# Kernel optimization log

Measured on AMD Instinct MI355X. Metric: run time of the kernel, lower is better.

## Reference

```python
import jax, jax.numpy as jnp
import numpy as np

N = 50000
E = 800000
D_IN = 64
D_E = 32
H = 128
EPS = 1e-5


def _seg_mean(msgs, dst, n):
    s = jax.ops.segment_sum(msgs, dst, num_segments=n)
    c = jax.ops.segment_sum(jnp.ones((dst.shape[0], 1), msgs.dtype), dst, num_segments=n)
    return s / jnp.maximum(c, 1.0)


def _bn(h, g, b, m, v):
    return g * (h - m) * jax.lax.rsqrt(v + EPS) + b


def setup_inputs() -> dict:
    key = jax.random.key(0)
    ks = jax.random.split(key, 32)
    inp = {
        "x": jax.random.normal(ks[0], (N, D_IN), jnp.float32),
        "edge_index_0": jax.random.randint(ks[1], (2, E), 0, N),
        "edge_index_1": jax.random.randint(ks[2], (2, E), 0, N),
        "edge_index_2": jax.random.randint(ks[3], (2, E), 0, N),
        "edge_attr_0": jax.random.normal(ks[4], (E, D_E), jnp.float32),
        # conv1: Linear(D_IN + D_E -> H)
        "W1": jax.random.normal(ks[5], (H, D_IN + D_E), jnp.float32) * 0.1,
        "b1": jnp.zeros((H,), jnp.float32),
        "g1": jnp.ones((H,), jnp.float32), "be1": jnp.zeros((H,), jnp.float32),
        "m1": jax.random.normal(ks[6], (H,), jnp.float32) * 0.1,
        "v1": jax.random.uniform(ks[7], (H,), jnp.float32) + 0.5,
        # SAGEConv2: lin_l (bias) on aggregated neighbors + lin_r (no bias) on self
        "Wl2": jax.random.normal(ks[8], (H, H), jnp.float32) * 0.1,
        "bl2": jnp.zeros((H,), jnp.float32),
        "Wr2": jax.random.normal(ks[9], (H, H), jnp.float32) * 0.1,
        "g2": jnp.ones((H,), jnp.float32), "be2": jnp.zeros((H,), jnp.float32),
        "m2": jax.random.normal(ks[10], (H,), jnp.float32) * 0.1,
        "v2": jax.random.uniform(ks[11], (H,), jnp.float32) + 0.5,
        # SAGEConv3
        "Wl3": jax.random.normal(ks[12], (H, H), jnp.float32) * 0.1,
        "bl3": jnp.zeros((H,), jnp.float32),
        "Wr3": jax.random.normal(ks[13], (H, H), jnp.float32) * 0.1,
        "g3": jnp.ones((H,), jnp.float32), "be3": jnp.zeros((H,), jnp.float32),
        "m3": jax.random.normal(ks[14], (H,), jnp.float32) * 0.1,
        "v3": jax.random.uniform(ks[15], (H,), jnp.float32) + 0.5,
        # mlp: Linear(H + D_IN -> 64) -> ReLU -> Linear(64 -> 1)
        "W4": jax.random.normal(ks[16], (64, H + D_IN), jnp.float32) * 0.1,
        "b4": jnp.zeros((64,), jnp.float32),
        "W5": jax.random.normal(ks[17], (1, 64), jnp.float32) * 0.1,
        "b5": jnp.zeros((1,), jnp.float32),
    }
    return inp


def reference(x, edge_index_0, edge_index_1, edge_index_2, edge_attr_0,
              W1, b1, g1, be1, m1, v1,
              Wl2, bl2, Wr2, g2, be2, m2, v2,
              Wl3, bl3, Wr3, g3, be3, m3, v3,
              W4, b4, W5, b5):
    n = x.shape[0]
    init = x
    # conv1: gather x_j + edge_attr, concat, linear, mean scatter, relu (update)
    msg = jnp.concatenate([x[edge_index_0[0]], edge_attr_0], axis=-1) @ W1.T + b1  # [E,H]
    h = jax.nn.relu(_seg_mean(msg, edge_index_0[1], n))
    h = jax.nn.relu(_bn(h, g1, be1, m1, v1))  # dropout: eval (identity)
    # conv2: SAGEConv = lin_l(mean_j x_j) + lin_r(x)
    agg = _seg_mean(h[edge_index_1[0]], edge_index_1[1], n)
    h = agg @ Wl2.T + bl2 + h @ Wr2.T
    h = jax.nn.relu(_bn(h, g2, be2, m2, v2))
    # conv3
    agg = _seg_mean(h[edge_index_2[0]], edge_index_2[1], n)
    h = agg @ Wl3.T + bl3 + h @ Wr3.T
    h = jax.nn.relu(_bn(h, g3, be3, m3, v3))
    # readout mlp on [h, initial_embedding]
    z = jnp.concatenate([h, init], axis=1)
    z = jax.nn.relu(z @ W4.T + b4)
    out = (z @ W5.T + b5).squeeze(-1)  # [N]
    return out
```

## Files before the change

### kernel.cpp

```cpp
#include <hip/hip_runtime.h>
#include <hip/hip_bf16.h>
#include <stdint.h>

#define NN 50000
#define NE 800000
#define EPS 1e-5f

#define KB 196
#define SH 8
#define NPB 256
#define RCAP 4500
#define PT2 2048

typedef __attribute__((ext_vector_type(8))) short bf16x8;
typedef __attribute__((ext_vector_type(4))) float floatx4;

static __device__ __forceinline__ float bf2f(unsigned int u){
  union { unsigned int i; float f; } c; c.i = u << 16; return c.f;
}
static __device__ __forceinline__ unsigned short f2bf(float f){
  union { float f; unsigned int i; } c; c.f = f;
  unsigned int x = c.i;
  return (unsigned short)((x + 0x7fffu + ((x >> 16) & 1u)) >> 16);
}

#define CVT_X   3200000
#define CVT_W1  3212288
#define CVT_WL2 3228672
#define CVT_WR2 3245056
#define CVT_WL3 3261440
#define CVT_WR3 3277824
#define CVT_END 3290112
__global__ void k_cvt_all(const float* __restrict__ x,  const float* __restrict__ W1,
                          const float* __restrict__ Wl2, const float* __restrict__ Wr2,
                          const float* __restrict__ Wl3, const float* __restrict__ Wr3,
                          const float* __restrict__ W4,
                          unsigned short* __restrict__ xb,  unsigned short* __restrict__ W1b,
                          unsigned short* __restrict__ Wl2b, unsigned short* __restrict__ Wr2b,
                          unsigned short* __restrict__ Wl3b, unsigned short* __restrict__ Wr3b,
                          unsigned short* __restrict__ W4b, int* __restrict__ gcur){
  int i = blockIdx.x * 256 + threadIdx.x;
  if(i >= CVT_END) return;
  if(i < 3 * KB) gcur[i] = 0;
  if(i < CVT_X)        xb[i] = f2bf(x[i]);
  else if(i < CVT_W1)  W1b[i - CVT_X]    = f2bf(W1[i - CVT_X]);
  else if(i < CVT_WL2) Wl2b[i - CVT_W1]  = f2bf(Wl2[i - CVT_W1]);
  else if(i < CVT_WR2) Wr2b[i - CVT_WL2] = f2bf(Wr2[i - CVT_WL2]);
  else if(i < CVT_WL3) Wl3b[i - CVT_WR2] = f2bf(Wl3[i - CVT_WR2]);
  else if(i < CVT_WR3) Wr3b[i - CVT_WL3] = f2bf(Wr3[i - CVT_WL3]);
  else                 W4b[i - CVT_WR3]  = f2bf(W4[i - CVT_WR3]);
}

__global__ void k_part0(const int* __restrict__ ei, int* __restrict__ gcur,
                        int2* __restrict__ rec, int* __restrict__ recE){
  __shared__ int2 stage[PT2];
  __shared__ int stE[PT2];
  __shared__ int hist[KB], ex[KB], cur[KB], gbase[KB];
  __shared__ int part[256];
  __shared__ int tot;
  int tid = threadIdx.x;
  int tile = blockIdx.x * PT2;
  for(int i = tid; i < KB; i += 256) hist[i] = 0;
  __syncthreads();
  int dst[8], src[8];
  #pragma unroll
  for(int j = 0; j < 8; j++){
    int e = tile + j * 256 + tid;
    if(e < NE){ src[j] = ei[e]; dst[j] = ei[NE + e]; atomicAdd(&hist[dst[j] >> SH], 1); }
    else dst[j] = -1;
  }
  __syncthreads();
  int c0 = (tid < KB) ? hist[tid] : 0;
  part[tid] = c0;
  __syncthreads();
  for(int d = 1; d < 256; d <<= 1){
    int v = (tid >= d) ? part[tid - d] : 0;
    __syncthreads();
    part[tid] += v;
    __syncthreads();
  }
  if(tid < KB){
    int e = part[tid] - c0;
    ex[tid] = e; cur[tid] = e;
    gbase[tid] = atomicAdd(&gcur[tid], c0);
  }
  if(tid == 255) tot = part[255];
  __syncthreads();
  #pragma unroll
  for(int j = 0; j < 8; j++){
    if(dst[j] >= 0){
      int b = dst[j] >> SH;
      int s = atomicAdd(&cur[b], 1);
      stage[s] = make_int2(dst[j], src[j]);
      stE[s] = tile + j * 256 + tid;
    }
  }
  __syncthreads();
  for(int s = tid; s < tot; s += 256){
    int2 r = stage[s];
    int b = r.x >> SH;
    int idx = b * RCAP + gbase[b] + (s - ex[b]);
    rec[idx] = r;
    recE[idx] = stE[s];
  }
}

__global__ void k_part(const int* __restrict__ ei, int* __restrict__ gcur, int2* __restrict__ rec){
  __shared__ int2 stage[PT2];
  __shared__ int hist[KB], ex[KB], cur[KB], gbase[KB];
  __shared__ int part[256];
  __shared__ int tot;
  int tid = threadIdx.x;
  int tile = blockIdx.x * PT2;
  for(int i = tid; i < KB; i += 256) hist[i] = 0;
  __syncthreads();
  int dst[8], src[8];
  #pragma unroll
  for(int j = 0; j < 8; j++){
    int e = tile + j * 256 + tid;
    if(e < NE){ src[j] = ei[e]; dst[j] = ei[NE + e]; atomicAdd(&hist[dst[j] >> SH], 1); }
    else dst[j] = -1;
  }
  __syncthreads();
  int c0 = (tid < KB) ? hist[tid] : 0;
  part[tid] = c0;
  __syncthreads();
  for(int d = 1; d < 256; d <<= 1){
    int v = (tid >= d) ? part[tid - d] : 0;
    __syncthreads();
    part[tid] += v;
    __syncthreads();
  }
  if(tid < KB){
    int e = part[tid] - c0;
    ex[tid] = e; cur[tid] = e;
    gbase[tid] = atomicAdd(&gcur[tid], c0);
  }
  if(tid == 255) tot = part[255];
  __syncthreads();
  #pragma unroll
  for(int j = 0; j < 8; j++){
    if(dst[j] >= 0){
      int b = dst[j] >> SH;
      int s = atomicAdd(&cur[b], 1);
      stage[s] = make_int2(dst[j], src[j]);
    }
  }
  __syncthreads();
  for(int s = tid; s < tot; s += 256){
    int2 r = stage[s];
    int b = r.x >> SH;
    rec[b * RCAP + gbase[b] + (s - ex[b])] = r;
  }
}

__global__ void k_build0(const int2* __restrict__ rec, const int* __restrict__ recE,
                         const int* __restrict__ gcnt,
                         int2* __restrict__ adj2, int* __restrict__ rowbeg, int* __restrict__ deg){
  __shared__ int cnt[NPB], cur2[NPB];
  __shared__ int part[256];
  int b = blockIdx.x, tid = threadIdx.x;
  int n0 = b << SH;
  int nr = gcnt[b];
  const int2* r = rec + b * RCAP;
  const int* re = recE + b * RCAP;
  cnt[tid] = 0;
  __syncthreads();
  for(int k = tid; k < nr; k += 256) atomicAdd(&cnt[r[k].x - n0], 1);
  __syncthreads();
  int c0 = cnt[tid];
  part[tid] = c0;
  __syncthreads();
  for(int d = 1; d < 256; d <<= 1){
    int v = (tid >= d) ? part[tid - d] : 0;
    __syncthreads();
    part[tid] += v;
    __syncthreads();
  }
  int base = part[tid] - c0;
  cur2[tid] = base;
  __syncthreads();
  int n = n0 + tid;
  if(n < NN){ rowbeg[n] = b * RCAP + base; deg[n] = c0; }
  for(int k = tid; k < nr; k += 256){
    int2 q = r[k];
    int p = atomicAdd(&cur2[q.x - n0], 1);
    adj2[b * RCAP + p] = make_int2(q.y, re[k]);
  }
}

__global__ void k_build(const int2* __restrict__ rec, const int* __restrict__ gcnt,
                        int* __restrict__ adj, int* __restrict__ rowbeg, int* __restrict__ deg){
  __shared__ int cnt[NPB], cur2[NPB];
  __shared__ int part[256];
  int b = blockIdx.x, tid = threadIdx.x;
  int n0 = b << SH;
  int nr = gcnt[b];
  const int2* r = rec + b * RCAP;
  cnt[tid] = 0;
  __syncthreads();
  for(int k = tid; k < nr; k += 256) atomicAdd(&cnt[r[k].x - n0], 1);
  __syncthreads();
  int c0 = cnt[tid];
  part[tid] = c0;
  __syncthreads();
  for(int d = 1; d < 256; d <<= 1){
    int v = (tid >= d) ? part[tid - d] : 0;
    __syncthreads();
    part[tid] += v;
    __syncthreads();
  }
  int base = part[tid] - c0;
  cur2[tid] = base;
  __syncthreads();
  int n = n0 + tid;
  if(n < NN){ rowbeg[n] = b * RCAP + base; deg[n] = c0; }
  for(int k = tid; k < nr; k += 256){
    int2 q = r[k];
    int p = atomicAdd(&cur2[q.x - n0], 1);
    adj[b * RCAP + p] = q.y;
  }
}

__global__ void k_aggXE(const int* __restrict__ rowbeg, const int* __restrict__ deg,
                        const int2* __restrict__ adj2,
                        const unsigned short* __restrict__ xb, const float* __restrict__ ea,
                        unsigned short* __restrict__ agg){
  int w = (blockIdx.x * blockDim.x + threadIdx.x) >> 6;
  int lane = threadIdx.x & 63;
  if(w >= NN) return;
  int sub = lane >> 4, li = lane & 15;
  int r0 = rowbeg[w], dg = deg[w], r1 = r0 + dg;
  float acc[8] = {0.f,0.f,0.f,0.f,0.f,0.f,0.f,0.f};
  for(int k = r0; k < r1; k += 8){
    int e0 = k + sub, e1 = k + 4 + sub;
    int i0 = e0 < r1 ? e0 : r1 - 1;
    int i1 = e1 < r1 ? e1 : r1 - 1;
    float m0 = e0 < r1 ? 1.f : 0.f;
    float m1 = e1 < r1 ? 1.f : 0.f;
    int2 a0 = adj2[i0], a1 = adj2[i1];
    if(li < 8){
      uint4 v0 = *(const uint4*)(xb + (size_t)a0.x * 64 + li * 8);
      uint4 v1 = *(const uint4*)(xb + (size_t)a1.x * 64 + li * 8);
      acc[0] += m0 * bf2f(v0.x & 0xffffu); acc[1] += m0 * bf2f(v0.x >> 16);
      acc[2] += m0 * bf2f(v0.y & 0xffffu); acc[3] += m0 * bf2f(v0.y >> 16);
      acc[4] += m0 * bf2f(v0.z & 0xffffu); acc[5] += m0 * bf2f(v0.z >> 16);
      acc[6] += m0 * bf2f(v0.w & 0xffffu); acc[7] += m0 * bf2f(v0.w >> 16);
      acc[0] += m1 * bf2f(v1.x & 0xffffu); acc[1] += m1 * bf2f(v1.x >> 16);
      acc[2] += m1 * bf2f(v1.y & 0xffffu); acc[3] += m1 * bf2f(v1.y >> 16);
      acc[4] += m1 * bf2f(v1.z & 0xffffu); acc[5] += m1 * bf2f(v1.z >> 16);
      acc[6] += m1 * bf2f(v1.w & 0xffffu); acc[7] += m1 * bf2f(v1.w >> 16);
    } else {
      int j = li - 8;
      float4 p0 = *(const float4*)(ea + (size_t)a0.y * 32 + j * 4);
      float4 p1 = *(const float4*)(ea + (size_t)a1.y * 32 + j * 4);
      acc[0] += m0 * p0.x; acc[1] += m0 * p0.y;
      acc[2] += m0 * p0.z; acc[3] += m0 * p0.w;
      acc[0] += m1 * p1.x; acc[1] += m1 * p1.y;
      acc[2] += m1 * p1.z; acc[3] += m1 * p1.w;
    }
  }
  #pragma unroll
  for(int d = 16; d < 64; d <<= 1){
    #pragma unroll
    for(int i = 0; i < 8; i++) acc[i] += __shfl_xor(acc[i], d, 64);
  }
  if(sub == 0){
    float inv = 1.0f / (float)(dg > 0 ? dg : 1);
    if(li < 8){
      unsigned int q0 = (unsigned int)f2bf(acc[0]*inv) | ((unsigned int)f2bf(acc[1]*inv) << 16);
      unsigned int q1 = (unsigned int)f2bf(acc[2]*inv) | ((unsigned int)f2bf(acc[3]*inv) << 16);
      unsigned int q2 = (unsigned int)f2bf(acc[4]*inv) | ((unsigned int)f2bf(acc[5]*inv) << 16);
      unsigned int q3 = (unsigned int)f2bf(acc[6]*inv) | ((unsigned int)f2bf(acc[7]*inv) << 16);
      *(uint4*)(agg + (size_t)w * 96 + li * 8) = make_uint4(q0, q1, q2, q3);
    } else {
      int j = li - 8;
      unsigned int q0 = (unsigned int)f2bf(acc[0]*inv) | ((unsigned int)f2bf(acc[1]*inv) << 16);
      unsigned int q1 = (unsigned int)f2bf(acc[2]*inv) | ((unsigned int)f2bf(acc[3]*inv) << 16);
      *(uint2*)(agg + (size_t)w * 96 + 64 + j * 4) = make_uint2(q0, q1);
    }
  }
}

__global__ void k_aggH(const int* __restrict__ rowbeg, const int* __restrict__ deg,
                       const int* __restrict__ adj,
                       const unsigned short* __restrict__ h, unsigned short* __restrict__ agg){
  int w = (blockIdx.x * blockDim.x + threadIdx.x) >> 6;
  int lane = threadIdx.x & 63;
  if(w >= NN) return;
  int sub = lane >> 4, li = lane & 15;
  int r0 = rowbeg[w], dg = deg[w], r1 = r0 + dg;
  float acc[8] = {0.f,0.f,0.f,0.f,0.f,0.f,0.f,0.f};
  for(int k = r0; k < r1; k += 8){
    int e0 = k + sub, e1 = k + 4 + sub;
    int i0 = e0 < r1 ? e0 : r1 - 1;
    int i1 = e1 < r1 ? e1 : r1 - 1;
    float m0 = e0 < r1 ? 1.f : 0.f;
    float m1 = e1 < r1 ? 1.f : 0.f;
    int s0 = adj[i0], s1 = adj[i1];
    uint4 v0 = *(const uint4*)(h + (size_t)s0 * 128 + li * 8);
    uint4 v1 = *(const uint4*)(h + (size_t)s1 * 128 + li * 8);
    acc[0] += m0 * bf2f(v0.x & 0xffffu); acc[1] += m0 * bf2f(v0.x >> 16);
    acc[2] += m0 * bf2f(v0.y & 0xffffu); acc[3] += m0 * bf2f(v0.y >> 16);
    acc[4] += m0 * bf2f(v0.z & 0xffffu); acc[5] += m0 * bf2f(v0.z >> 16);
    acc[6] += m0 * bf2f(v0.w & 0xffffu); acc[7] += m0 * bf2f(v0.w >> 16);
    acc[0] += m1 * bf2f(v1.x & 0xffffu); acc[1] += m1 * bf2f(v1.x >> 16);
    acc[2] += m1 * bf2f(v1.y & 0xffffu); acc[3] += m1 * bf2f(v1.y >> 16);
    acc[4] += m1 * bf2f(v1.z & 0xffffu); acc[5] += m1 * bf2f(v1.z >> 16);
    acc[6] += m1 * bf2f(v1.w & 0xffffu); acc[7] += m1 * bf2f(v1.w >> 16);
  }
  #pragma unroll
  for(int d = 16; d < 64; d <<= 1){
    #pragma unroll
    for(int i = 0; i < 8; i++) acc[i] += __shfl_xor(acc[i], d, 64);
  }
  if(sub == 0){
    float inv = 1.0f / (float)(dg > 0 ? dg : 1);
    unsigned int p0 = (unsigned int)f2bf(acc[0]*inv) | ((unsigned int)f2bf(acc[1]*inv) << 16);
    unsigned int p1 = (unsigned int)f2bf(acc[2]*inv) | ((unsigned int)f2bf(acc[3]*inv) << 16);
    unsigned int p2 = (unsigned int)f2bf(acc[4]*inv) | ((unsigned int)f2bf(acc[5]*inv) << 16);
    unsigned int p3 = (unsigned int)f2bf(acc[6]*inv) | ((unsigned int)f2bf(acc[7]*inv) << 16);
    *(uint4*)(agg + (size_t)w * 128 + li * 8) = make_uint4(p0, p1, p2, p3);
  }
}

__global__ void k_lin1(const unsigned short* __restrict__ agg, const unsigned short* __restrict__ W1,
                       const float* __restrict__ b1,
                       const float* __restrict__ g1, const float* __restrict__ be1,
                       const float* __restrict__ m1, const float* __restrict__ v1,
                       const int* __restrict__ deg, unsigned short* __restrict__ h1){
  int wave = (blockIdx.x * blockDim.x + threadIdx.x) >> 6;
  int lane = threadIdx.x & 63;
  int mt = wave >> 3, nt = wave & 7;
  if(mt >= 3125) return;
  int node0 = mt * 16;
  int col = lane & 15, quad = lane >> 4;
  int o = nt * 16 + col;
  int arow = node0 + col;
  floatx4 acc = {0.f, 0.f, 0.f, 0.f};
  #pragma unroll
  for(int kc = 0; kc < 3; kc++){
    bf16x8 a = *(const bf16x8*)(agg + arow * 96 + kc * 32 + quad * 8);
    bf16x8 b = *(const bf16x8*)(W1 + o * 96 + kc * 32 + quad * 8);
    acc = __builtin_amdgcn_mfma_f32_16x16x32_bf16(a, b, acc, 0, 0, 0);
  }
  float bb = b1[o];
  float sc = g1[o] * rsqrtf(v1[o] + EPS);
  float mv = m1[o], bev = be1[o];
  #pragma unroll
  for(int r = 0; r < 4; r++){
    int node = node0 + quad * 4 + r;
    float pre = (deg[node] > 0) ? (acc[r] + bb) : 0.0f;
    float t = fmaxf(pre, 0.f);
    float bn = sc * (t - mv) + bev;
    h1[node * 128 + o] = f2bf(fmaxf(bn, 0.f));
  }
}

__global__ void k_sage(const unsigned short* __restrict__ agg, const unsigned short* __restrict__ hin,
                       const unsigned short* __restrict__ Wl, const float* __restrict__ bl,
                       const unsigned short* __restrict__ Wr,
                       const float* __restrict__ g, const float* __restrict__ be,
                       const float* __restrict__ m, const float* __restrict__ v,
                       unsigned short* __restrict__ hout){
  int wave = (blockIdx.x * blockDim.x + threadIdx.x) >> 6;
  int lane = threadIdx.x & 63;
  int mt = wave >> 3, nt = wave & 7;
  if(mt >= 3125) return;
  int node0 = mt * 16;
  int col = lane & 15, quad = lane >> 4;
  int o = nt * 16 + col;
  int arow = node0 + col;
  floatx4 acc = {0.f, 0.f, 0.f, 0.f};
  #pragma unroll
  for(int kc = 0; kc < 4; kc++){
    bf16x8 a = *(const bf16x8*)(agg + arow * 128 + kc * 32 + quad * 8);
    bf16x8 b = *(const bf16x8*)(Wl + o * 128 + kc * 32 + quad * 8);
    acc = __builtin_amdgcn_mfma_f32_16x16x32_bf16(a, b, acc, 0, 0, 0);
  }
  #pragma unroll
  for(int kc = 0; kc < 4; kc++){
    bf16x8 a = *(const bf16x8*)(hin + arow * 128 + kc * 32 + quad * 8);
    bf16x8 b = *(const bf16x8*)(Wr + o * 128 + kc * 32 + quad * 8);
    acc = __builtin_amdgcn_mfma_f32_16x16x32_bf16(a, b, acc, 0, 0, 0);
  }
  float blv = bl[o];
  float sc = g[o] * rsqrtf(v[o] + EPS);
  float mv = m[o], bev = be[o];
  #pragma unroll
  for(int r = 0; r < 4; r++){
    int node = node0 + quad * 4 + r;
    float pre = acc[r] + blv;
    float bn = sc * (pre - mv) + bev;
    hout[node * 128 + o] = f2bf(fmaxf(bn, 0.f));
  }
}

__global__ void k_readout(const unsigned short* __restrict__ h3, const unsigned short* __restrict__ xb,
                          const unsigned short* __restrict__ W4, const float* __restrict__ b4,
                          const float* __restrict__ W5, const float* __restrict__ b5,
                          float* __restrict__ out){
  int wave = (blockIdx.x * blockDim.x + threadIdx.x) >> 6;
  int lane = threadIdx.x & 63;
  if(wave >= 3125) return;
  int node0 = wave * 16;
  int col = lane & 15, quad = lane >> 4;
  int arow = node0 + col;
  float partial[4] = {0.f, 0.f, 0.f, 0.f};
  #pragma unroll
  for(int nt = 0; nt < 4; nt++){
    int o = nt * 16 + col;
    floatx4 acc = {0.f, 0.f, 0.f, 0.f};
    #pragma unroll
    for(int kc = 0; kc < 4; kc++){
      bf16x8 a = *(const bf16x8*)(h3 + arow * 128 + kc * 32 + quad * 8);
      bf16x8 b = *(const bf16x8*)(W4 + o * 192 + kc * 32 + quad * 8);
      acc = __builtin_amdgcn_mfma_f32_16x16x32_bf16(a, b, acc, 0, 0, 0);
    }
    #pragma unroll
    for(int kc = 0; kc < 2; kc++){
      bf16x8 a = *(const bf16x8*)(xb + arow * 64 + kc * 32 + quad * 8);
      bf16x8 b = *(const bf16x8*)(W4 + o * 192 + 128 + kc * 32 + quad * 8);
      acc = __builtin_amdgcn_mfma_f32_16x16x32_bf16(a, b, acc, 0, 0, 0);
    }
    float bb = b4[o];
    float w5 = W5[o];
    #pragma unroll
    for(int r = 0; r < 4; r++)
      partial[r] += fmaxf(acc[r] + bb, 0.f) * w5;
  }
  #pragma unroll
  for(int d = 1; d < 16; d <<= 1){
    #pragma unroll
    for(int r = 0; r < 4; r++)
      partial[r] += __shfl_xor(partial[r], d, 64);
  }
  if(col == 0){
    float b5f = b5[0];
    #pragma unroll
    for(int r = 0; r < 4; r++)
      out[node0 + quad * 4 + r] = partial[r] + b5f;
  }
}

extern "C" void kernel_launch(void* const* d_in, const int* in_sizes, int n_in,
                              void* d_out, int out_size, void* d_ws, size_t ws_size,
                              hipStream_t stream) {
  const float* x   = (const float*)d_in[0];
  const int* ei0   = (const int*)d_in[1];
  const int* ei1   = (const int*)d_in[2];
  const int* ei2   = (const int*)d_in[3];
  const float* ea  = (const float*)d_in[4];
  const float* W1  = (const float*)d_in[5];
  const float* b1  = (const float*)d_in[6];
  const float* g1  = (const float*)d_in[7];
  const float* be1 = (const float*)d_in[8];
  const float* m1  = (const float*)d_in[9];
  const float* v1  = (const float*)d_in[10];
  const float* Wl2 = (const float*)d_in[11];
  const float* bl2 = (const float*)d_in[12];
  const float* Wr2 = (const float*)d_in[13];
  const float* g2  = (const float*)d_in[14];
  const float* be2 = (const float*)d_in[15];
  const float* m2  = (const float*)d_in[16];
  const float* v2  = (const float*)d_in[17];
  const float* Wl3 = (const float*)d_in[18];
  const float* bl3 = (const float*)d_in[19];
  const float* Wr3 = (const float*)d_in[20];
  const float* g3  = (const float*)d_in[21];
  const float* be3 = (const float*)d_in[22];
  const float* m3  = (const float*)d_in[23];
  const float* v3  = (const float*)d_in[24];
  const float* W4  = (const float*)d_in[25];
  const float* b4  = (const float*)d_in[26];
  const float* W5  = (const float*)d_in[27];
  const float* b5  = (const float*)d_in[28];

  char* ws = (char*)d_ws;
  size_t off = 0;
  auto alloc = [&](size_t bytes) -> void* {
    void* p = (void*)(ws + off);
    off += (bytes + 255) & ~(size_t)255;
    return p;
  };
  int* gcur    = (int*)alloc(3 * KB * sizeof(int));
  int* rowbeg3 = (int*)alloc(3 * NN * sizeof(int));
  int* deg3    = (int*)alloc(3 * NN * sizeof(int));
  int2* recDS  = (int2*)alloc((size_t)KB * RCAP * 8);
  int2* adj2   = (int2*)alloc((size_t)KB * RCAP * 8);
  unsigned short* hbuf = (unsigned short*)alloc((size_t)KB * RCAP * 64);
  unsigned short* agg1 = (unsigned short*)alloc((size_t)NN * 96 * 2);
  unsigned short* xb   = (unsigned short*)alloc((size_t)NN * 64 * 2);
  unsigned short* W1b  = (unsigned short*)alloc(12288 * 2);
  unsigned short* Wl2b = (unsigned short*)alloc(16384 * 2);
  unsigned short* Wr2b = (unsigned short*)alloc(16384 * 2);
  unsigned short* Wl3b = (unsigned short*)alloc(16384 * 2);
  unsigned short* Wr3b = (unsigned short*)alloc(16384 * 2);
  unsigned short* W4b  = (unsigned short*)alloc(12288 * 2);

  int* adjI = (int*)adj2;

  unsigned short* h1   = hbuf;
  unsigned short* aggH = h1 + (size_t)NN * 128;
  unsigned short* h2   = h1 + (size_t)2 * NN * 128;
  unsigned short* h3   = h1 + (size_t)3 * NN * 128;
  int* recE = (int*)((char*)hbuf + (size_t)4 * NN * 128 * 2);

  int* rb0 = rowbeg3;            int* dg0 = deg3;
  int* rb1 = rowbeg3 + NN;       int* dg1 = deg3 + NN;
  int* rb2 = rowbeg3 + 2 * NN;   int* dg2 = deg3 + 2 * NN;

  const int gP2   = (NE + PT2 - 1) / PT2;
  const int gAgg  = (NN * 64) / 256;
  const int gTile = (3125 * 8 * 64) / 256;
  const int gRead = (3125 * 64 + 255) / 256;
  const int gCvt  = (CVT_END + 255) / 256;

  k_cvt_all<<<gCvt, 256, 0, stream>>>(x, W1, Wl2, Wr2, Wl3, Wr3, W4,
                                      xb, W1b, Wl2b, Wr2b, Wl3b, Wr3b, W4b, gcur);

  k_part0<<<gP2, 256, 0, stream>>>(ei0, gcur, recDS, recE);
  k_build0<<<KB, 256, 0, stream>>>(recDS, recE, gcur, adj2, rb0, dg0);
  k_aggXE<<<gAgg, 256, 0, stream>>>(rb0, dg0, adj2, xb, ea, agg1);
  k_lin1<<<gTile, 256, 0, stream>>>(agg1, W1b, b1, g1, be1, m1, v1, dg0, h1);

  k_part<<<gP2, 256, 0, stream>>>(ei1, gcur + KB, recDS);
  k_build<<<KB, 256, 0, stream>>>(recDS, gcur + KB, adjI, rb1, dg1);
  k_aggH<<<gAgg, 256, 0, stream>>>(rb1, dg1, adjI, h1, aggH);
  k_sage<<<gTile, 256, 0, stream>>>(aggH, h1, Wl2b, bl2, Wr2b, g2, be2, m2, v2, h2);

  k_part<<<gP2, 256, 0, stream>>>(ei2, gcur + 2 * KB, recDS);
  k_build<<<KB, 256, 0, stream>>>(recDS, gcur + 2 * KB, adjI, rb2, dg2);
  k_aggH<<<gAgg, 256, 0, stream>>>(rb2, dg2, adjI, h2, aggH);
  k_sage<<<gTile, 256, 0, stream>>>(aggH, h2, Wl3b, bl3, Wr3b, g3, be3, m3, v3, h3);

  k_readout<<<gRead, 256, 0, stream>>>(h3, xb, W4b, b4, W5, b5, (float*)d_out);

  (void)in_sizes; (void)n_in; (void)out_size; (void)ws_size;
}
```

Before: 533.7 us.

## Scatter-add edge attributes with atomics and drop edge-id tracking in CSR build

Edge-attribute sums for conv1 are now computed by a separate coalesced pass that atomically adds each edge's 32 floats into a per-node fp32 buffer, zeroed during conversion. The edge-id array and the int2 adjacency for layer 0 go away, so the generic partition and build kernels are reused and aggregation only gathers bf16 x rows. The conv1 gather now covers 8 edges per step instead of 4, and the SAGE gather unrolls to 4 loads in flight per lane. The cost is 25.6M float atomics to global memory, and the edge-attribute sums now depend on atomic ordering.

```diff
diff --git a/kernel.cpp b/kernel.cpp
--- a/kernel.cpp
+++ b/kernel.cpp
@@ -38,10 +38,12 @@
                           unsigned short* __restrict__ xb,  unsigned short* __restrict__ W1b,
                           unsigned short* __restrict__ Wl2b, unsigned short* __restrict__ Wr2b,
                           unsigned short* __restrict__ Wl3b, unsigned short* __restrict__ Wr3b,
-                          unsigned short* __restrict__ W4b, int* __restrict__ gcur){
+                          unsigned short* __restrict__ W4b, int* __restrict__ gcur,
+                          float* __restrict__ aggE){
   int i = blockIdx.x * 256 + threadIdx.x;
   if(i >= CVT_END) return;
   if(i < 3 * KB) gcur[i] = 0;
+  if(i < NN * 32) aggE[i] = 0.f;
   if(i < CVT_X)        xb[i] = f2bf(x[i]);
   else if(i < CVT_W1)  W1b[i - CVT_X]    = f2bf(W1[i - CVT_X]);
   else if(i < CVT_WL2) Wl2b[i - CVT_W1]  = f2bf(Wl2[i - CVT_W1]);
@@ -51,58 +53,18 @@
   else                 W4b[i - CVT_WR3]  = f2bf(W4[i - CVT_WR3]);
 }
 
-__global__ void k_part0(const int* __restrict__ ei, int* __restrict__ gcur,
-                        int2* __restrict__ rec, int* __restrict__ recE){
-  __shared__ int2 stage[PT2];
-  __shared__ int stE[PT2];
-  __shared__ int hist[KB], ex[KB], cur[KB], gbase[KB];
-  __shared__ int part[256];
-  __shared__ int tot;
-  int tid = threadIdx.x;
-  int tile = blockIdx.x * PT2;
-  for(int i = tid; i < KB; i += 256) hist[i] = 0;
-  __syncthreads();
-  int dst[8], src[8];
-  #pragma unroll
-  for(int j = 0; j < 8; j++){
-    int e = tile + j * 256 + tid;
-    if(e < NE){ src[j] = ei[e]; dst[j] = ei[NE + e]; atomicAdd(&hist[dst[j] >> SH], 1); }
-    else dst[j] = -1;
-  }
-  __syncthreads();
-  int c0 = (tid < KB) ? hist[tid] : 0;
-  part[tid] = c0;
-  __syncthreads();
-  for(int d = 1; d < 256; d <<= 1){
-    int v = (tid >= d) ? part[tid - d] : 0;
-    __syncthreads();
-    part[tid] += v;
-    __syncthreads();
-  }
-  if(tid < KB){
-    int e = part[tid] - c0;
-    ex[tid] = e; cur[tid] = e;
-    gbase[tid] = atomicAdd(&gcur[tid], c0);
-  }
-  if(tid == 255) tot = part[255];
-  __syncthreads();
-  #pragma unroll
-  for(int j = 0; j < 8; j++){
-    if(dst[j] >= 0){
-      int b = dst[j] >> SH;
-      int s = atomicAdd(&cur[b], 1);
-      stage[s] = make_int2(dst[j], src[j]);
-      stE[s] = tile + j * 256 + tid;
-    }
-  }
-  __syncthreads();
-  for(int s = tid; s < tot; s += 256){
-    int2 r = stage[s];
-    int b = r.x >> SH;
-    int idx = b * RCAP + gbase[b] + (s - ex[b]);
-    rec[idx] = r;
-    recE[idx] = stE[s];
-  }
+__global__ void k_sumEA(const int* __restrict__ ei, const float* __restrict__ ea,
+                        float* __restrict__ aggE){
+  int t = blockIdx.x * 256 + threadIdx.x;
+  int e = t >> 3, li = t & 7;
+  if(e >= NE) return;
+  int dst = ei[NE + e];
+  float4 v = *(const float4*)(ea + (size_t)e * 32 + li * 4);
+  float* p = aggE + (size_t)dst * 32 + li * 4;
+  atomicAdd(p + 0, v.x);
+  atomicAdd(p + 1, v.y);
+  atomicAdd(p + 2, v.z);
+  atomicAdd(p + 3, v.w);
 }
 
 __global__ void k_part(const int* __restrict__ ei, int* __restrict__ gcur, int2* __restrict__ rec){
@@ -151,41 +113,6 @@
     int2 r = stage[s];
     int b = r.x >> SH;
     rec[b * RCAP + gbase[b] + (s - ex[b])] = r;
-  }
-}
-
-__global__ void k_build0(const int2* __restrict__ rec, const int* __restrict__ recE,
-                         const int* __restrict__ gcnt,
-                         int2* __restrict__ adj2, int* __restrict__ rowbeg, int* __restrict__ deg){
-  __shared__ int cnt[NPB], cur2[NPB];
-  __shared__ int part[256];
-  int b = blockIdx.x, tid = threadIdx.x;
-  int n0 = b << SH;
-  int nr = gcnt[b];
-  const int2* r = rec + b * RCAP;
-  const int* re = recE + b * RCAP;
-  cnt[tid] = 0;
-  __syncthreads();
-  for(int k = tid; k < nr; k += 256) atomicAdd(&cnt[r[k].x - n0], 1);
-  __syncthreads();
-  int c0 = cnt[tid];
-  part[tid] = c0;
-  __syncthreads();
-  for(int d = 1; d < 256; d <<= 1){
-    int v = (tid >= d) ? part[tid - d] : 0;
-    __syncthreads();
-    part[tid] += v;
-    __syncthreads();
-  }
-  int base = part[tid] - c0;
-  cur2[tid] = base;
-  __syncthreads();
-  int n = n0 + tid;
-  if(n < NN){ rowbeg[n] = b * RCAP + base; deg[n] = c0; }
-  for(int k = tid; k < nr; k += 256){
-    int2 q = r[k];
-    int p = atomicAdd(&cur2[q.x - n0], 1);
-    adj2[b * RCAP + p] = make_int2(q.y, re[k]);
   }
 }
 
@@ -223,62 +150,51 @@
 }
 
 __global__ void k_aggXE(const int* __restrict__ rowbeg, const int* __restrict__ deg,
-                        const int2* __restrict__ adj2,
-                        const unsigned short* __restrict__ xb, const float* __restrict__ ea,
+                        const int* __restrict__ adj,
+                        const unsigned short* __restrict__ xb, const float* __restrict__ aggE,
                         unsigned short* __restrict__ agg){
   int w = (blockIdx.x * blockDim.x + threadIdx.x) >> 6;
   int lane = threadIdx.x & 63;
   if(w >= NN) return;
-  int sub = lane >> 4, li = lane & 15;
+  int sub = lane >> 3, li = lane & 7;
   int r0 = rowbeg[w], dg = deg[w], r1 = r0 + dg;
   float acc[8] = {0.f,0.f,0.f,0.f,0.f,0.f,0.f,0.f};
-  for(int k = r0; k < r1; k += 8){
-    int e0 = k + sub, e1 = k + 4 + sub;
+  for(int k = r0; k < r1; k += 16){
+    int e0 = k + sub, e1 = k + 8 + sub;
     int i0 = e0 < r1 ? e0 : r1 - 1;
     int i1 = e1 < r1 ? e1 : r1 - 1;
     float m0 = e0 < r1 ? 1.f : 0.f;
     float m1 = e1 < r1 ? 1.f : 0.f;
-    int2 a0 = adj2[i0], a1 = adj2[i1];
-    if(li < 8){
-      uint4 v0 = *(const uint4*)(xb + (size_t)a0.x * 64 + li * 8);
-      uint4 v1 = *(const uint4*)(xb + (size_t)a1.x * 64 + li * 8);
-      acc[0] += m0 * bf2f(v0.x & 0xffffu); acc[1] += m0 * bf2f(v0.x >> 16);
-      acc[2] += m0 * bf2f(v0.y & 0xffffu); acc[3] += m0 * bf2f(v0.y >> 16);
-      acc[4] += m0 * bf2f(v0.z & 0xffffu); acc[5] += m0 * bf2f(v0.z >> 16);
-      acc[6] += m0 * bf2f(v0.w & 0xffffu); acc[7] += m0 * bf2f(v0.w >> 16);
-      acc[0] += m1 * bf2f(v1.x & 0xffffu); acc[1] += m1 * bf2f(v1.x >> 16);
-      acc[2] += m1 * bf2f(v1.y & 0xffffu); acc[3] += m1 * bf2f(v1.y >> 16);
-      acc[4] += m1 * bf2f(v1.z & 0xffffu); acc[5] += m1 * bf2f(v1.z >> 16);
-      acc[6] += m1 * bf2f(v1.w & 0xffffu); acc[7] += m1 * bf2f(v1.w >> 16);
-    } else {
-      int j = li - 8;
-      float4 p0 = *(const float4*)(ea + (size_t)a0.y * 32 + j * 4);
-      float4 p1 = *(const float4*)(ea + (size_t)a1.y * 32 + j * 4);
-      acc[0] += m0 * p0.x; acc[1] += m0 * p0.y;
-      acc[2] += m0 * p0.z; acc[3] += m0 * p0.w;
-      acc[0] += m1 * p1.x; acc[1] += m1 * p1.y;
-      acc[2] += m1 * p1.z; acc[3] += m1 * p1.w;
-    }
-  }
-  #pragma unroll
-  for(int d = 16; d < 64; d <<= 1){
+    int s0 = adj[i0], s1 = adj[i1];
+    uint4 v0 = *(const uint4*)(xb + (size_t)s0 * 64 + li * 8);
+    uint4 v1 = *(const uint4*)(xb + (size_t)s1 * 64 + li * 8);
+    acc[0] += m0 * bf2f(v0.x & 0xffffu); acc[1] += m0 * bf2f(v0.x >> 16);
+    acc[2] += m0 * bf2f(v0.y & 0xffffu); acc[3] += m0 * bf2f(v0.y >> 16);
+    acc[4] += m0 * bf2f(v0.z & 0xffffu); acc[5] += m0 * bf2f(v0.z >> 16);
+    acc[6] += m0 * bf2f(v0.w & 0xffffu); acc[7] += m0 * bf2f(v0.w >> 16);
+    acc[0] += m1 * bf2f(v1.x & 0xffffu); acc[1] += m1 * bf2f(v1.x >> 16);
+    acc[2] += m1 * bf2f(v1.y & 0xffffu); acc[3] += m1 * bf2f(v1.y >> 16);
+    acc[4] += m1 * bf2f(v1.z & 0xffffu); acc[5] += m1 * bf2f(v1.z >> 16);
+    acc[6] += m1 * bf2f(v1.w & 0xffffu); acc[7] += m1 * bf2f(v1.w >> 16);
+  }
+  #pragma unroll
+  for(int d = 8; d < 64; d <<= 1){
     #pragma unroll
     for(int i = 0; i < 8; i++) acc[i] += __shfl_xor(acc[i], d, 64);
   }
-  if(sub == 0){
-    float inv = 1.0f / (float)(dg > 0 ? dg : 1);
-    if(li < 8){
-      unsigned int q0 = (unsigned int)f2bf(acc[0]*inv) | ((unsigned int)f2bf(acc[1]*inv) << 16);
-      unsigned int q1 = (unsigned int)f2bf(acc[2]*inv) | ((unsigned int)f2bf(acc[3]*inv) << 16);
-      unsigned int q2 = (unsigned int)f2bf(acc[4]*inv) | ((unsigned int)f2bf(acc[5]*inv) << 16);
-      unsigned int q3 = (unsigned int)f2bf(acc[6]*inv) | ((unsigned int)f2bf(acc[7]*inv) << 16);
-      *(uint4*)(agg + (size_t)w * 96 + li * 8) = make_uint4(q0, q1, q2, q3);
-    } else {
-      int j = li - 8;
-      unsigned int q0 = (unsigned int)f2bf(acc[0]*inv) | ((unsigned int)f2bf(acc[1]*inv) << 16);
-      unsigned int q1 = (unsigned int)f2bf(acc[2]*inv) | ((unsigned int)f2bf(acc[3]*inv) << 16);
-      *(uint2*)(agg + (size_t)w * 96 + 64 + j * 4) = make_uint2(q0, q1);
-    }
+  float inv = 1.0f / (float)(dg > 0 ? dg : 1);
+  if(lane < 8){
+    unsigned int q0 = (unsigned int)f2bf(acc[0]*inv) | ((unsigned int)f2bf(acc[1]*inv) << 16);
+    unsigned int q1 = (unsigned int)f2bf(acc[2]*inv) | ((unsigned int)f2bf(acc[3]*inv) << 16);
+    unsigned int q2 = (unsigned int)f2bf(acc[4]*inv) | ((unsigned int)f2bf(acc[5]*inv) << 16);
+    unsigned int q3 = (unsigned int)f2bf(acc[6]*inv) | ((unsigned int)f2bf(acc[7]*inv) << 16);
+    *(uint4*)(agg + (size_t)w * 96 + lane * 8) = make_uint4(q0, q1, q2, q3);
+  } else if(lane < 16){
+    int j = lane - 8;
+    float4 s = *(const float4*)(aggE + (size_t)w * 32 + j * 4);
+    unsigned int q0 = (unsigned int)f2bf(s.x*inv) | ((unsigned int)f2bf(s.y*inv) << 16);
+    unsigned int q1 = (unsigned int)f2bf(s.z*inv) | ((unsigned int)f2bf(s.w*inv) << 16);
+    *(uint2*)(agg + (size_t)w * 96 + 64 + j * 4) = make_uint2(q0, q1);
   }
 }
 
@@ -291,23 +207,23 @@
   int sub = lane >> 4, li = lane & 15;
   int r0 = rowbeg[w], dg = deg[w], r1 = r0 + dg;
   float acc[8] = {0.f,0.f,0.f,0.f,0.f,0.f,0.f,0.f};
-  for(int k = r0; k < r1; k += 8){
-    int e0 = k + sub, e1 = k + 4 + sub;
-    int i0 = e0 < r1 ? e0 : r1 - 1;
-    int i1 = e1 < r1 ? e1 : r1 - 1;
-    float m0 = e0 < r1 ? 1.f : 0.f;
-    float m1 = e1 < r1 ? 1.f : 0.f;
-    int s0 = adj[i0], s1 = adj[i1];
-    uint4 v0 = *(const uint4*)(h + (size_t)s0 * 128 + li * 8);
-    uint4 v1 = *(const uint4*)(h + (size_t)s1 * 128 + li * 8);
-    acc[0] += m0 * bf2f(v0.x & 0xffffu); acc[1] += m0 * bf2f(v0.x >> 16);
-    acc[2] += m0 * bf2f(v0.y & 0xffffu); acc[3] += m0 * bf2f(v0.y >> 16);
-    acc[4] += m0 * bf2f(v0.z & 0xffffu); acc[5] += m0 * bf2f(v0.z >> 16);
-    acc[6] += m0 * bf2f(v0.w & 0xffffu); acc[7] += m0 * bf2f(v0.w >> 16);
-    acc[0] += m1 * bf2f(v1.x & 0xffffu); acc[1] += m1 * bf2f(v1.x >> 16);
-    acc[2] += m1 * bf2f(v1.y & 0xffffu); acc[3] += m1 * bf2f(v1.y >> 16);
-    acc[4] += m1 * bf2f(v1.z & 0xffffu); acc[5] += m1 * bf2f(v1.z >> 16);
-    acc[6] += m1 * bf2f(v1.w & 0xffffu); acc[7] += m1 * bf2f(v1.w >> 16);
+  for(int k = r0; k < r1; k += 16){
+    uint4 v[4]; float msk[4];
+    #pragma unroll
+    for(int u = 0; u < 4; u++){
+      int e = k + u * 4 + sub;
+      int i = e < r1 ? e : r1 - 1;
+      msk[u] = e < r1 ? 1.f : 0.f;
+      int s = adj[i];
+      v[u] = *(const uint4*)(h + (size_t)s * 128 + li * 8);
+    }
+    #pragma unroll
+    for(int u = 0; u < 4; u++){
+      acc[0] += msk[u] * bf2f(v[u].x & 0xffffu); acc[1] += msk[u] * bf2f(v[u].x >> 16);
+      acc[2] += msk[u] * bf2f(v[u].y & 0xffffu); acc[3] += msk[u] * bf2f(v[u].y >> 16);
+      acc[4] += msk[u] * bf2f(v[u].z & 0xffffu); acc[5] += msk[u] * bf2f(v[u].z >> 16);
+      acc[6] += msk[u] * bf2f(v[u].w & 0xffffu); acc[7] += msk[u] * bf2f(v[u].w >> 16);
+    }
   }
   #pragma unroll
   for(int d = 16; d < 64; d <<= 1){
@@ -487,8 +403,9 @@
   int* rowbeg3 = (int*)alloc(3 * NN * sizeof(int));
   int* deg3    = (int*)alloc(3 * NN * sizeof(int));
   int2* recDS  = (int2*)alloc((size_t)KB * RCAP * 8);
-  int2* adj2   = (int2*)alloc((size_t)KB * RCAP * 8);
-  unsigned short* hbuf = (unsigned short*)alloc((size_t)KB * RCAP * 64);
+  int* adjI    = (int*)alloc((size_t)KB * RCAP * 4);
+  float* aggE  = (float*)alloc((size_t)NN * 32 * 4);
+  unsigned short* hbuf = (unsigned short*)alloc((size_t)4 * NN * 128 * 2);
   unsigned short* agg1 = (unsigned short*)alloc((size_t)NN * 96 * 2);
   unsigned short* xb   = (unsigned short*)alloc((size_t)NN * 64 * 2);
   unsigned short* W1b  = (unsigned short*)alloc(12288 * 2);
@@ -498,30 +415,29 @@
   unsigned short* Wr3b = (unsigned short*)alloc(16384 * 2);
   unsigned short* W4b  = (unsigned short*)alloc(12288 * 2);
 
-  int* adjI = (int*)adj2;
-
   unsigned short* h1   = hbuf;
   unsigned short* aggH = h1 + (size_t)NN * 128;
   unsigned short* h2   = h1 + (size_t)2 * NN * 128;
   unsigned short* h3   = h1 + (size_t)3 * NN * 128;
-  int* recE = (int*)((char*)hbuf + (size_t)4 * NN * 128 * 2);
 
   int* rb0 = rowbeg3;            int* dg0 = deg3;
   int* rb1 = rowbeg3 + NN;       int* dg1 = deg3 + NN;
   int* rb2 = rowbeg3 + 2 * NN;   int* dg2 = deg3 + 2 * NN;
 
   const int gP2   = (NE + PT2 - 1) / PT2;
+  const int gSum  = (NE * 8) / 256;
   const int gAgg  = (NN * 64) / 256;
   const int gTile = (3125 * 8 * 64) / 256;
   const int gRead = (3125 * 64 + 255) / 256;
   const int gCvt  = (CVT_END + 255) / 256;
 
   k_cvt_all<<<gCvt, 256, 0, stream>>>(x, W1, Wl2, Wr2, Wl3, Wr3, W4,
-                                      xb, W1b, Wl2b, Wr2b, Wl3b, Wr3b, W4b, gcur);
-
-  k_part0<<<gP2, 256, 0, stream>>>(ei0, gcur, recDS, recE);
-  k_build0<<<KB, 256, 0, stream>>>(recDS, recE, gcur, adj2, rb0, dg0);
-  k_aggXE<<<gAgg, 256, 0, stream>>>(rb0, dg0, adj2, xb, ea, agg1);
+                                      xb, W1b, Wl2b, Wr2b, Wl3b, Wr3b, W4b, gcur, aggE);
+
+  k_sumEA<<<gSum, 256, 0, stream>>>(ei0, ea, aggE);
+  k_part<<<gP2, 256, 0, stream>>>(ei0, gcur, recDS);
+  k_build<<<KB, 256, 0, stream>>>(recDS, gcur, adjI, rb0, dg0);
+  k_aggXE<<<gAgg, 256, 0, stream>>>(rb0, dg0, adjI, xb, aggE, agg1);
   k_lin1<<<gTile, 256, 0, stream>>>(agg1, W1b, b1, g1, be1, m1, v1, dg0, h1);
 
   k_part<<<gP2, 256, 0, stream>>>(ei1, gcur + KB, recDS);
```

After: 806.9 us. +51.2%, slower.

## Batch CSR partition and build for all three layers into single launches

Applied to the files above, without the earlier changes.

The per-layer partition and CSR-build kernels are merged into k_part3 and k_build3, which use blockIdx modulo 3 to select the layer, so all three graphs are preprocessed in two launches instead of six. Each layer now gets its own adjacency array, and the workspace is re-laid out so the staging records alias the hidden-state buffers, with h3 reusing h1. The aim is to cut launch and tail overhead and fill the GPU with more blocks per launch. The cost is larger workspace for the separate adjacency arrays and some fragile buffer aliasing.

```diff
diff --git a/kernel.cpp b/kernel.cpp
--- a/kernel.cpp
+++ b/kernel.cpp
@@ -11,6 +11,7 @@
 #define NPB 256
 #define RCAP 4500
 #define PT2 2048
+#define NT2 391
 
 typedef __attribute__((ext_vector_type(8))) short bf16x8;
 typedef __attribute__((ext_vector_type(4))) float floatx4;
@@ -51,15 +52,20 @@
   else                 W4b[i - CVT_WR3]  = f2bf(W4[i - CVT_WR3]);
 }
 
-__global__ void k_part0(const int* __restrict__ ei, int* __restrict__ gcur,
+__global__ void k_part3(const int* __restrict__ ei0, const int* __restrict__ ei1,
+                        const int* __restrict__ ei2, int* __restrict__ gcur,
                         int2* __restrict__ rec, int* __restrict__ recE){
   __shared__ int2 stage[PT2];
   __shared__ int stE[PT2];
   __shared__ int hist[KB], ex[KB], cur[KB], gbase[KB];
   __shared__ int part[256];
   __shared__ int tot;
+  int layer = blockIdx.x % 3;
+  int tile = (blockIdx.x / 3) * PT2;
+  const int* ei = (layer == 0) ? ei0 : ((layer == 1) ? ei1 : ei2);
+  int2* recL = rec + (size_t)layer * KB * RCAP;
+  int* gcurL = gcur + layer * KB;
   int tid = threadIdx.x;
-  int tile = blockIdx.x * PT2;
   for(int i = tid; i < KB; i += 256) hist[i] = 0;
   __syncthreads();
   int dst[8], src[8];
@@ -82,7 +88,7 @@
   if(tid < KB){
     int e = part[tid] - c0;
     ex[tid] = e; cur[tid] = e;
-    gbase[tid] = atomicAdd(&gcur[tid], c0);
+    gbase[tid] = atomicAdd(&gcurL[tid], c0);
   }
   if(tid == 255) tot = part[255];
   __syncthreads();
@@ -92,7 +98,7 @@
       int b = dst[j] >> SH;
       int s = atomicAdd(&cur[b], 1);
       stage[s] = make_int2(dst[j], src[j]);
-      stE[s] = tile + j * 256 + tid;
+      if(layer == 0) stE[s] = tile + j * 256 + tid;
     }
   }
   __syncthreads();
@@ -100,29 +106,29 @@
     int2 r = stage[s];
     int b = r.x >> SH;
     int idx = b * RCAP + gbase[b] + (s - ex[b]);
-    rec[idx] = r;
-    recE[idx] = stE[s];
-  }
-}
-
-__global__ void k_part(const int* __restrict__ ei, int* __restrict__ gcur, int2* __restrict__ rec){
-  __shared__ int2 stage[PT2];
-  __shared__ int hist[KB], ex[KB], cur[KB], gbase[KB];
+    recL[idx] = r;
+    if(layer == 0) recE[idx] = stE[s];
+  }
+}
+
+__global__ void k_build3(const int2* __restrict__ rec, const int* __restrict__ recE,
+                         const int* __restrict__ gcnt,
+                         int2* __restrict__ adj2, int* __restrict__ adjI1, int* __restrict__ adjI2,
+                         int* __restrict__ rowbeg3, int* __restrict__ deg3){
+  __shared__ int cnt[NPB], cur2[NPB];
   __shared__ int part[256];
-  __shared__ int tot;
+  int layer = blockIdx.x % 3;
+  int b = blockIdx.x / 3;
   int tid = threadIdx.x;
-  int tile = blockIdx.x * PT2;
-  for(int i = tid; i < KB; i += 256) hist[i] = 0;
-  __syncthreads();
-  int dst[8], src[8];
-  #pragma unroll
-  for(int j = 0; j < 8; j++){
-    int e = tile + j * 256 + tid;
-    if(e < NE){ src[j] = ei[e]; dst[j] = ei[NE + e]; atomicAdd(&hist[dst[j] >> SH], 1); }
-    else dst[j] = -1;
-  }
-  __syncthreads();
-  int c0 = (tid < KB) ? hist[tid] : 0;
+  int n0 = b << SH;
+  int nr = gcnt[layer * KB + b];
+  const int2* r = rec + ((size_t)layer * KB + b) * RCAP;
+  const int* re = recE + (size_t)b * RCAP;
+  cnt[tid] = 0;
+  __syncthreads();
+  for(int k = tid; k < nr; k += 256) atomicAdd(&cnt[r[k].x - n0], 1);
+  __syncthreads();
+  int c0 = cnt[tid];
   part[tid] = c0;
   __syncthreads();
   for(int d = 1; d < 256; d <<= 1){
@@ -131,94 +137,17 @@
     part[tid] += v;
     __syncthreads();
   }
-  if(tid < KB){
-    int e = part[tid] - c0;
-    ex[tid] = e; cur[tid] = e;
-    gbase[tid] = atomicAdd(&gcur[tid], c0);
-  }
-  if(tid == 255) tot = part[255];
-  __syncthreads();
-  #pragma unroll
-  for(int j = 0; j < 8; j++){
-    if(dst[j] >= 0){
-      int b = dst[j] >> SH;
-      int s = atomicAdd(&cur[b], 1);
-      stage[s] = make_int2(dst[j], src[j]);
-    }
-  }
-  __syncthreads();
-  for(int s = tid; s < tot; s += 256){
-    int2 r = stage[s];
-    int b = r.x >> SH;
-    rec[b * RCAP + gbase[b] + (s - ex[b])] = r;
-  }
-}
-
-__global__ void k_build0(const int2* __restrict__ rec, const int* __restrict__ recE,
-                         const int* __restrict__ gcnt,
-                         int2* __restrict__ adj2, int* __restrict__ rowbeg, int* __restrict__ deg){
-  __shared__ int cnt[NPB], cur2[NPB];
-  __shared__ int part[256];
-  int b = blockIdx.x, tid = threadIdx.x;
-  int n0 = b << SH;
-  int nr = gcnt[b];
-  const int2* r = rec + b * RCAP;
-  const int* re = recE + b * RCAP;
-  cnt[tid] = 0;
-  __syncthreads();
-  for(int k = tid; k < nr; k += 256) atomicAdd(&cnt[r[k].x - n0], 1);
-  __syncthreads();
-  int c0 = cnt[tid];
-  part[tid] = c0;
-  __syncthreads();
-  for(int d = 1; d < 256; d <<= 1){
-    int v = (tid >= d) ? part[tid - d] : 0;
-    __syncthreads();
-    part[tid] += v;
-    __syncthreads();
-  }
   int base = part[tid] - c0;
   cur2[tid] = base;
   __syncthreads();
   int n = n0 + tid;
-  if(n < NN){ rowbeg[n] = b * RCAP + base; deg[n] = c0; }
+  if(n < NN){ rowbeg3[layer * NN + n] = b * RCAP + base; deg3[layer * NN + n] = c0; }
   for(int k = tid; k < nr; k += 256){
     int2 q = r[k];
     int p = atomicAdd(&cur2[q.x - n0], 1);
-    adj2[b * RCAP + p] = make_int2(q.y, re[k]);
-  }
-}
-
-__global__ void k_build(const int2* __restrict__ rec, const int* __restrict__ gcnt,
-                        int* __restrict__ adj, int* __restrict__ rowbeg, int* __restrict__ deg){
-  __shared__ int cnt[NPB], cur2[NPB];
-  __shared__ int part[256];
-  int b = blockIdx.x, tid = threadIdx.x;
-  int n0 = b << SH;
-  int nr = gcnt[b];
-  const int2* r = rec + b * RCAP;
-  cnt[tid] = 0;
-  __syncthreads();
-  for(int k = tid; k < nr; k += 256) atomicAdd(&cnt[r[k].x - n0], 1);
-  __syncthreads();
-  int c0 = cnt[tid];
-  part[tid] = c0;
-  __syncthreads();
-  for(int d = 1; d < 256; d <<= 1){
-    int v = (tid >= d) ? part[tid - d] : 0;
-    __syncthreads();
-    part[tid] += v;
-    __syncthreads();
-  }
-  int base = part[tid] - c0;
-  cur2[tid] = base;
-  __syncthreads();
-  int n = n0 + tid;
-  if(n < NN){ rowbeg[n] = b * RCAP + base; deg[n] = c0; }
-  for(int k = tid; k < nr; k += 256){
-    int2 q = r[k];
-    int p = atomicAdd(&cur2[q.x - n0], 1);
-    adj[b * RCAP + p] = q.y;
+    if(layer == 0)      adj2[b * RCAP + p]  = make_int2(q.y, re[k]);
+    else if(layer == 1) adjI1[b * RCAP + p] = q.y;
+    else                adjI2[b * RCAP + p] = q.y;
   }
 }
 
@@ -486,9 +415,10 @@
   int* gcur    = (int*)alloc(3 * KB * sizeof(int));
   int* rowbeg3 = (int*)alloc(3 * NN * sizeof(int));
   int* deg3    = (int*)alloc(3 * NN * sizeof(int));
-  int2* recDS  = (int2*)alloc((size_t)KB * RCAP * 8);
+  char* uni    = (char*)alloc((size_t)3 * NN * 128 * 2);
   int2* adj2   = (int2*)alloc((size_t)KB * RCAP * 8);
-  unsigned short* hbuf = (unsigned short*)alloc((size_t)KB * RCAP * 64);
+  int* adjI1   = (int*)alloc((size_t)KB * RCAP * 4);
+  int* adjI2   = (int*)alloc((size_t)KB * RCAP * 4);
   unsigned short* agg1 = (unsigned short*)alloc((size_t)NN * 96 * 2);
   unsigned short* xb   = (unsigned short*)alloc((size_t)NN * 64 * 2);
   unsigned short* W1b  = (unsigned short*)alloc(12288 * 2);
@@ -498,19 +428,19 @@
   unsigned short* Wr3b = (unsigned short*)alloc(16384 * 2);
   unsigned short* W4b  = (unsigned short*)alloc(12288 * 2);
 
-  int* adjI = (int*)adj2;
-
-  unsigned short* h1   = hbuf;
+  int2* recDS = (int2*)uni;
+  int* recE   = (int*)(uni + (((size_t)3 * KB * RCAP * 8 + 255) & ~(size_t)255));
+  unsigned short* h1   = (unsigned short*)uni;
   unsigned short* aggH = h1 + (size_t)NN * 128;
   unsigned short* h2   = h1 + (size_t)2 * NN * 128;
-  unsigned short* h3   = h1 + (size_t)3 * NN * 128;
-  int* recE = (int*)((char*)hbuf + (size_t)4 * NN * 128 * 2);
+  unsigned short* h3   = h1;
 
   int* rb0 = rowbeg3;            int* dg0 = deg3;
   int* rb1 = rowbeg3 + NN;       int* dg1 = deg3 + NN;
   int* rb2 = rowbeg3 + 2 * NN;   int* dg2 = deg3 + 2 * NN;
 
-  const int gP2   = (NE + PT2 - 1) / PT2;
+  const int gP3   = 3 * NT2;
+  const int gB3   = 3 * KB;
   const int gAgg  = (NN * 64) / 256;
   const int gTile = (3125 * 8 * 64) / 256;
   const int gRead = (3125 * 64 + 255) / 256;
@@ -519,19 +449,16 @@
   k_cvt_all<<<gCvt, 256, 0, stream>>>(x, W1, Wl2, Wr2, Wl3, Wr3, W4,
                                       xb, W1b, Wl2b, Wr2b, Wl3b, Wr3b, W4b, gcur);
 
-  k_part0<<<gP2, 256, 0, stream>>>(ei0, gcur, recDS, recE);
-  k_build0<<<KB, 256, 0, stream>>>(recDS, recE, gcur, adj2, rb0, dg0);
+  k_part3<<<gP3, 256, 0, stream>>>(ei0, ei1, ei2, gcur, recDS, recE);
+  k_build3<<<gB3, 256, 0, stream>>>(recDS, recE, gcur, adj2, adjI1, adjI2, rowbeg3, deg3);
+
   k_aggXE<<<gAgg, 256, 0, stream>>>(rb0, dg0, adj2, xb, ea, agg1);
   k_lin1<<<gTile, 256, 0, stream>>>(agg1, W1b, b1, g1, be1, m1, v1, dg0, h1);
 
-  k_part<<<gP2, 256, 0, stream>>>(ei1, gcur + KB, recDS);
-  k_build<<<KB, 256, 0, stream>>>(recDS, gcur + KB, adjI, rb1, dg1);
-  k_aggH<<<gAgg, 256, 0, stream>>>(rb1, dg1, adjI, h1, aggH);
+  k_aggH<<<gAgg, 256, 0, stream>>>(rb1, dg1, adjI1, h1, aggH);
   k_sage<<<gTile, 256, 0, stream>>>(aggH, h1, Wl2b, bl2, Wr2b, g2, be2, m2, v2, h2);
 
-  k_part<<<gP2, 256, 0, stream>>>(ei2, gcur + 2 * KB, recDS);
-  k_build<<<KB, 256, 0, stream>>>(recDS, gcur + 2 * KB, adjI, rb2, dg2);
-  k_aggH<<<gAgg, 256, 0, stream>>>(rb2, dg2, adjI, h2, aggH);
+  k_aggH<<<gAgg, 256, 0, stream>>>(rb2, dg2, adjI2, h2, aggH);
   k_sage<<<gTile, 256, 0, stream>>>(aggH, h2, Wl3b, bl3, Wr3b, g3, be3, m3, v3, h3);
 
   k_readout<<<gRead, 256, 0, stream>>>(h3, xb, W4b, b4, W5, b5, (float*)d_out);
```

Measured after the change: 491.3 us. 7.9% less time.
